# Optimization experiments

Measured on AMD Instinct MI355X. Metric: run time of the kernel, lower is better.

The kernel has to match this reference:

```python
import jax, jax.numpy as jnp
import numpy as np

EPS = 1e-5

def _ln(x, g, b):
    m = jnp.mean(x, -1, keepdims=True)
    v = jnp.var(x, -1, keepdims=True)
    return (x - m) / jnp.sqrt(v + EPS) * g + b

def _rel_shift(x):
    # x: [B, qlen, klen, n_head] -- TransformerXL relative shift
    b, q, k, n = x.shape
    xp = jnp.pad(x, ((0, 0), (0, 0), (1, 0), (0, 0)))  # zero-pad along klen front
    xp = xp.reshape(b, k + 1, q, n)[:, 1:]
    return xp.reshape(b, q, k, n)

def setup_inputs() -> dict:
    key = jax.random.key(0)
    B, Q, D, N, DH, DI = 4, 1024, 1024, 16, 64, 4096
    ks = jax.random.split(key, 9)
    s = 0.02
    w = jax.random.normal(ks[0], (B, Q, D), jnp.float32)
    r = jax.random.normal(ks[1], (1, Q, D), jnp.float32)
    attention_mask = jnp.triu(jnp.ones((Q, Q), bool), k=1)  # 1 == masked (causal)
    qkv_w = jax.random.normal(ks[2], (3 * D, D), jnp.float32) * s
    r_w = jax.random.normal(ks[3], (D, D), jnp.float32) * s
    o_w = jax.random.normal(ks[4], (D, D), jnp.float32) * s
    r_w_bias = jax.random.normal(ks[5], (N, DH), jnp.float32) * s
    r_r_bias = jax.random.normal(ks[6], (N, DH), jnp.float32) * s
    ln1_g = jnp.ones(D, jnp.float32); ln1_b = jnp.zeros(D, jnp.float32)
    ff_w1 = jax.random.normal(ks[7], (DI, D), jnp.float32) * s
    ff_b1 = jnp.zeros(DI, jnp.float32)
    ff_w2 = jax.random.normal(ks[8], (D, DI), jnp.float32) * s
    ff_b2 = jnp.zeros(D, jnp.float32)
    ln2_g = jnp.ones(D, jnp.float32); ln2_b = jnp.zeros(D, jnp.float32)
    return dict(w=w, r=r, attention_mask=attention_mask, qkv_w=qkv_w, r_w=r_w,
                o_w=o_w, r_w_bias=r_w_bias, r_r_bias=r_r_bias, ln1_g=ln1_g,
                ln1_b=ln1_b, ff_w1=ff_w1, ff_b1=ff_b1, ff_w2=ff_w2, ff_b2=ff_b2,
                ln2_g=ln2_g, ln2_b=ln2_b)

def reference(w, r, attention_mask, qkv_w, r_w, o_w, r_w_bias, r_r_bias,
              ln1_g, ln1_b, ff_w1, ff_b1, ff_w2, ff_b2, ln2_g, ln2_b):
    B, Q, D = w.shape
    N, DH = r_w_bias.shape
    # QKV projection (post-lnorm path, no mem)
    heads = w @ qkv_w.T  # [B,Q,3D]
    q, k, v = jnp.split(heads, 3, axis=-1)
    q = q.reshape(B, Q, N, DH)
    k = k.reshape(B, Q, N, DH)
    v = v.reshape(B, Q, N, DH)
    rk = (r[0] @ r_w.T).reshape(Q, N, DH)  # [rlen,N,DH]
    # content (AC) and position (BD) terms, computed in fp32 as in original
    AC = jnp.einsum('bind,bjnd->bijn', q + r_w_bias, k)
    BD = _rel_shift(jnp.einsum('bind,jnd->bijn', q + r_r_bias, rk))
    score = (AC + BD) * (1.0 / jnp.sqrt(jnp.float32(DH)))
    score = jnp.where(attention_mask[None, :, :, None], -1e30, score)
    prob = jax.nn.softmax(score, axis=2)  # softmax over klen
    av = jnp.einsum('bijn,bjnd->bind', prob, v).reshape(B, Q, D)
    out1 = _ln(w + av @ o_w.T, ln1_g, ln1_b)  # deepnorm_alpha = 1.0
    ff = jax.nn.relu(out1 @ ff_w1.T + ff_b1) @ ff_w2.T + ff_b2
    return _ln(out1 + ff, ln2_g, ln2_b)
```

## Files before the change

kernel.cpp:

```cpp
#include <hip/hip_runtime.h>
#include <hip/hip_bf16.h>

typedef __attribute__((ext_vector_type(8))) short short8;
typedef __attribute__((ext_vector_type(4))) short short4v;
typedef __attribute__((ext_vector_type(4))) float floatx4;

__device__ inline float bs2f(short s) {
    unsigned int u = ((unsigned int)(unsigned short)s) << 16;
    float f; __builtin_memcpy(&f, &u, 4); return f;
}
__device__ inline short f2bs(float f) {
    __hip_bfloat16 h = __float2bfloat16(f);
    unsigned short u; __builtin_memcpy(&u, &h, 2); return (short)u;
}
__device__ inline float ldf(const float* p)           { return *p; }
__device__ inline float ldf(const __hip_bfloat16* p)  { return __bfloat162float(*p); }
__device__ inline void  stf(float* p, float v)          { *p = v; }
__device__ inline void  stf(__hip_bfloat16* p, float v) { *p = __float2bfloat16(v); }

__device__ inline void gl_lds16(const short* g, short* l) {
    __builtin_amdgcn_global_load_lds(
        (const __attribute__((address_space(1))) void*)g,
        (__attribute__((address_space(3))) void*)l, 16, 0, 0);
}

__global__ __launch_bounds__(256) void f2b_all_kernel(
    const float* __restrict__ s0, const float* __restrict__ s1,
    const float* __restrict__ s2, const float* __restrict__ s3,
    const float* __restrict__ s4, const float* __restrict__ s5,
    const float* __restrict__ s6, __hip_bfloat16* __restrict__ dst)
{
    const long id  = blockIdx.x;
    const long gid = id * 1024 + threadIdx.x * 4;
    const float* src; long base;
    if      (id < 4096)  { src = s0; base = 0; }
    else if (id < 5120)  { src = s1; base = 4096L  * 1024; }
    else if (id < 8192)  { src = s2; base = 5120L  * 1024; }
    else if (id < 9216)  { src = s3; base = 8192L  * 1024; }
    else if (id < 10240) { src = s4; base = 9216L  * 1024; }
    else if (id < 14336) { src = s5; base = 10240L * 1024; }
    else                 { src = s6; base = 14336L * 1024; }
    const float4 v = *(const float4*)(src + (gid - base));
    dst[gid + 0] = __float2bfloat16(v.x);
    dst[gid + 1] = __float2bfloat16(v.y);
    dst[gid + 2] = __float2bfloat16(v.z);
    dst[gid + 3] = __float2bfloat16(v.w);
}

__global__ __launch_bounds__(256, 2) void gemm128_nt_kernel(
    const __hip_bfloat16* __restrict__ A,
    const __hip_bfloat16* __restrict__ Bw,
    __hip_bfloat16* __restrict__ C,
    int M, int N, int K,
    const float* __restrict__ bias,
    int do_relu)
{
    __shared__ short lA[128 * 32];
    __shared__ short lB[128 * 32];

    const int lane = threadIdx.x & 63;
    const int w    = threadIdx.x >> 6;
    const int m16  = lane & 15;
    const int quad = lane >> 4;
    const int wr   = w >> 1, wc = w & 1;

    const long i0 = (long)blockIdx.y * 128;
    const long j0 = (long)blockIdx.x * 128;

    const short* Ap = (const short*)A;
    const short* Bp = (const short*)Bw;

    floatx4 acc[4][4];
    #pragma unroll
    for (int a = 0; a < 4; ++a)
        #pragma unroll
        for (int b = 0; b < 4; ++b) acc[a][b] = (floatx4){0.f, 0.f, 0.f, 0.f};

    const int srow = w * 32 + (lane >> 2);
    const int scol = (lane & 3) * 8;
    const short* ga = Ap + (i0 + srow) * K + scol;
    const short* gb = Bp + (j0 + srow) * K + scol;
    short* la = lA + (w * 32) * 32;
    short* lb = lB + (w * 32) * 32;

    for (int k0 = 0; k0 < K; k0 += 32) {
        __syncthreads();
        gl_lds16(ga + k0,            la);
        gl_lds16(ga + 16 * K + k0,   la + 16 * 32);
        gl_lds16(gb + k0,            lb);
        gl_lds16(gb + 16 * K + k0,   lb + 16 * 32);
        __syncthreads();

        short8 af[4], bf[4];
        #pragma unroll
        for (int rb = 0; rb < 4; ++rb)
            af[rb] = *(const short8*)&lA[(wr * 64 + rb * 16 + m16) * 32 + quad * 8];
        #pragma unroll
        for (int cb = 0; cb < 4; ++cb)
            bf[cb] = *(const short8*)&lB[(wc * 64 + cb * 16 + m16) * 32 + quad * 8];
        #pragma unroll
        for (int rb = 0; rb < 4; ++rb)
            #pragma unroll
            for (int cb = 0; cb < 4; ++cb)
                acc[rb][cb] = __builtin_amdgcn_mfma_f32_16x16x32_bf16(
                    af[rb], bf[cb], acc[rb][cb], 0, 0, 0);
    }

    #pragma unroll
    for (int cb = 0; cb < 4; ++cb) {
        const long j = j0 + wc * 64 + cb * 16 + m16;
        const float bv = bias ? bias[j] : 0.f;
        #pragma unroll
        for (int rb = 0; rb < 4; ++rb) {
            #pragma unroll
            for (int rr = 0; rr < 4; ++rr) {
                const long row = i0 + wr * 64 + rb * 16 + quad * 4 + rr;
                float v = acc[rb][cb][rr] + bv;
                if (do_relu) v = fmaxf(v, 0.f);
                C[row * N + j] = __float2bfloat16(v);
            }
        }
    }
}

__global__ __launch_bounds__(256, 2) void gemm128_splitk_kernel(
    const __hip_bfloat16* __restrict__ A,
    const __hip_bfloat16* __restrict__ Bw,
    __hip_bfloat16* __restrict__ C0,
    __hip_bfloat16* __restrict__ C1,
    int M, int N, int K)
{
    __shared__ short lA[128 * 32];
    __shared__ short lB[128 * 32];

    const int lane = threadIdx.x & 63;
    const int w    = threadIdx.x >> 6;
    const int m16  = lane & 15;
    const int quad = lane >> 4;
    const int wr   = w >> 1, wc = w & 1;

    const long i0 = (long)blockIdx.y * 128;
    const long j0 = (long)blockIdx.x * 128;
    const int  kz = blockIdx.z;
    const int  kbeg = kz * (K >> 1), kend = kbeg + (K >> 1);

    const short* Ap = (const short*)A;
    const short* Bp = (const short*)Bw;

    floatx4 acc[4][4];
    #pragma unroll
    for (int a = 0; a < 4; ++a)
        #pragma unroll
        for (int b = 0; b < 4; ++b) acc[a][b] = (floatx4){0.f, 0.f, 0.f, 0.f};

    const int srow = w * 32 + (lane >> 2);
    const int scol = (lane & 3) * 8;
    const short* ga = Ap + (i0 + srow) * K + scol;
    const short* gb = Bp + (j0 + srow) * K + scol;
    short* la = lA + (w * 32) * 32;
    short* lb = lB + (w * 32) * 32;

    for (int k0 = kbeg; k0 < kend; k0 += 32) {
        __syncthreads();
        gl_lds16(ga + k0,            la);
        gl_lds16(ga + 16 * K + k0,   la + 16 * 32);
        gl_lds16(gb + k0,            lb);
        gl_lds16(gb + 16 * K + k0,   lb + 16 * 32);
        __syncthreads();

        short8 af[4], bf[4];
        #pragma unroll
        for (int rb = 0; rb < 4; ++rb)
            af[rb] = *(const short8*)&lA[(wr * 64 + rb * 16 + m16) * 32 + quad * 8];
        #pragma unroll
        for (int cb = 0; cb < 4; ++cb)
            bf[cb] = *(const short8*)&lB[(wc * 64 + cb * 16 + m16) * 32 + quad * 8];
        #pragma unroll
        for (int rb = 0; rb < 4; ++rb)
            #pragma unroll
            for (int cb = 0; cb < 4; ++cb)
                acc[rb][cb] = __builtin_amdgcn_mfma_f32_16x16x32_bf16(
                    af[rb], bf[cb], acc[rb][cb], 0, 0, 0);
    }

    __hip_bfloat16* C = kz ? C1 : C0;
    #pragma unroll
    for (int cb = 0; cb < 4; ++cb) {
        const long j = j0 + wc * 64 + cb * 16 + m16;
        #pragma unroll
        for (int rb = 0; rb < 4; ++rb) {
            #pragma unroll
            for (int rr = 0; rr < 4; ++rr) {
                const long row = i0 + wr * 64 + rb * 16 + quad * 4 + rr;
                C[row * N + j] = __float2bfloat16(acc[rb][cb][rr]);
            }
        }
    }
}

__global__ __launch_bounds__(256, 2) void gemm_n64_nt_kernel(
    const __hip_bfloat16* __restrict__ A,
    const __hip_bfloat16* __restrict__ Bw,
    __hip_bfloat16* __restrict__ C,
    int M, int N, int K,
    const float* __restrict__ bias,
    int do_relu)
{
    __shared__ short lA[128 * 32];
    __shared__ short lB[64 * 32];

    const int lane = threadIdx.x & 63;
    const int w    = threadIdx.x >> 6;
    const int m16  = lane & 15;
    const int quad = lane >> 4;
    const int wr   = w >> 1, wc = w & 1;

    const long i0 = (long)blockIdx.y * 128;
    const long j0 = (long)blockIdx.x * 64;

    const short* Ap = (const short*)A;
    const short* Bp = (const short*)Bw;

    floatx4 acc[4][2];
    #pragma unroll
    for (int a = 0; a < 4; ++a)
        #pragma unroll
        for (int b = 0; b < 2; ++b) acc[a][b] = (floatx4){0.f, 0.f, 0.f, 0.f};

    const int srowA = w * 32 + (lane >> 2);
    const int srowB = w * 16 + (lane >> 2);
    const int scol  = (lane & 3) * 8;
    const short* ga = Ap + (i0 + srowA) * K + scol;
    const short* gb = Bp + (j0 + srowB) * K + scol;
    short* la = lA + (w * 32) * 32;
    short* lb = lB + (w * 16) * 32;

    for (int k0 = 0; k0 < K; k0 += 32) {
        __syncthreads();
        gl_lds16(ga + k0,            la);
        gl_lds16(ga + 16 * K + k0,   la + 16 * 32);
        gl_lds16(gb + k0,            lb);
        __syncthreads();

        short8 af[4], bf[2];
        #pragma unroll
        for (int rb = 0; rb < 4; ++rb)
            af[rb] = *(const short8*)&lA[(wr * 64 + rb * 16 + m16) * 32 + quad * 8];
        #pragma unroll
        for (int cb = 0; cb < 2; ++cb)
            bf[cb] = *(const short8*)&lB[(wc * 32 + cb * 16 + m16) * 32 + quad * 8];
        #pragma unroll
        for (int rb = 0; rb < 4; ++rb)
            #pragma unroll
            for (int cb = 0; cb < 2; ++cb)
                acc[rb][cb] = __builtin_amdgcn_mfma_f32_16x16x32_bf16(
                    af[rb], bf[cb], acc[rb][cb], 0, 0, 0);
    }

    #pragma unroll
    for (int cb = 0; cb < 2; ++cb) {
        const long j = j0 + wc * 32 + cb * 16 + m16;
        const float bv = bias ? bias[j] : 0.f;
        #pragma unroll
        for (int rb = 0; rb < 4; ++rb) {
            #pragma unroll
            for (int rr = 0; rr < 4; ++rr) {
                const long row = i0 + wr * 64 + rb * 16 + quad * 4 + rr;
                float v = acc[rb][cb][rr] + bv;
                if (do_relu) v = fmaxf(v, 0.f);
                C[row * N + j] = __float2bfloat16(v);
            }
        }
    }
}

__global__ __launch_bounds__(256) void kvpack_kernel(
    const __hip_bfloat16* __restrict__ heads,
    short* __restrict__ kp, short* __restrict__ vp)
{
    const int Q = 1024, TD = 3072;
    __shared__ short kt[64 * 72];
    __shared__ short vt[64 * 72];
    const int tid = threadIdx.x;
    const int t  = blockIdx.x;
    const int bn = blockIdx.y;
    const int n = bn & 15, b = bn >> 4;
    const int j0 = t * 64;

    const short* hp = (const short*)heads + ((long)(b * Q + j0)) * TD + n * 64;
    {
        const int r = tid >> 2, c0 = (tid & 3) * 16;
        const short* src = hp + (long)r * TD + c0;
        *(short8*)&kt[r * 72 + c0]     = *(const short8*)(src + 1024);
        *(short8*)&kt[r * 72 + c0 + 8] = *(const short8*)(src + 1024 + 8);
        *(short8*)&vt[r * 72 + c0]     = *(const short8*)(src + 2048);
        *(short8*)&vt[r * 72 + c0 + 8] = *(const short8*)(src + 2048 + 8);
    }
    __syncthreads();

    const int lane = tid & 63;
    const int m16 = lane & 15, quad = lane >> 4;
    const long fb = ((long)bn * 16 + t) * 4096;
    #pragma unroll
    for (int pass = 0; pass < 2; ++pass) {
        const int fi = (tid >> 6) + pass * 4;
        const int c = fi >> 2, cb = fi & 3;
        short8 kf = *(const short8*)&kt[(cb * 16 + m16) * 72 + c * 32 + quad * 8];
        *(short8*)(kp + fb + fi * 512 + lane * 8) = kf;
        short8 vf;
        #pragma unroll
        for (int u = 0; u < 8; ++u)
            vf[u] = vt[(c * 32 + quad * 8 + u) * 72 + cb * 16 + m16];
        *(short8*)(vp + fb + fi * 512 + lane * 8) = vf;
    }
}

__global__ __launch_bounds__(256) void rkpack_kernel(
    const __hip_bfloat16* __restrict__ rkb, short* __restrict__ rkp)
{
    const int m = blockIdx.x;
    const int tid = threadIdx.x;
    const short4v v = *(const short4v*)((const short*)rkb + m * 1024 + tid * 4);
    const int n = tid >> 4, d = (tid * 4) & 63;
    *(short4v*)(rkp + ((long)n * 1024 + m) * 64 + d) = v;
}

__global__ __launch_bounds__(256, 2) void fattn_kernel(
    const __hip_bfloat16* __restrict__ heads,
    const short* __restrict__ kp,
    const short* __restrict__ vp,
    const short* __restrict__ rkp,
    const float* __restrict__ rwb,
    const float* __restrict__ rrb,
    __hip_bfloat16* __restrict__ av)
{
    const int Q = 1024, TD = 3072, D = 1024;
    const int tid  = threadIdx.x;
    const int lane = tid & 63;
    const int w    = tid >> 6;
    const int m16  = lane & 15;
    const int quad = lane >> 4;
    const int id = blockIdx.x;
    const int r8 = id & 7;
    const int z  = (id >> 3) & 7;
    const int bn = ((id >> 6) << 3) | r8;
    const int n = bn & 15, b = bn >> 4;

    __shared__ short pbuf[4][16 * 68];
    short* pb = pbuf[w];

    const short* hp = (const short*)heads;

    struct KV { short8 k[8], v[8]; };

    #pragma unroll
    for (int phase = 0; phase < 2; ++phase) {
        const int qt  = phase ? (15 - z) : z;
        const int iw0 = qt * 64 + w * 16;

        short8 qwf[2], qrf[2];
        {
            const long qoff = ((long)(b * Q + iw0 + m16)) * TD + n * 64;
            #pragma unroll
            for (int c = 0; c < 2; ++c) {
                short8 qv = *(const short8*)(hp + qoff + c * 32 + quad * 8);
                #pragma unroll
                for (int u = 0; u < 8; ++u) {
                    const int d = c * 32 + quad * 8 + u;
                    const float f = bs2f(qv[u]);
                    qwf[c][u] = f2bs(f + rwb[n * 64 + d]);
                    qrf[c][u] = f2bs(f + rrb[n * 64 + d]);
                }
            }
        }

        floatx4 oacc[4];
        #pragma unroll
        for (int t = 0; t < 4; ++t) oacc[t] = (floatx4){0.f, 0.f, 0.f, 0.f};
        float lsum[4] = {0.f, 0.f, 0.f, 0.f};

        auto loadKV = [&](KV& f, int t) {
            const long fb = ((long)bn * 16 + t) * 4096 + lane * 8;
            #pragma unroll
            for (int fi = 0; fi < 8; ++fi) {
                f.k[fi] = *(const short8*)(kp + fb + fi * 512);
                f.v[fi] = *(const short8*)(vp + fb + fi * 512);
            }
        };

        auto computeT = [&](const KV& f, int t) {
            const int j0 = t * 64;

            short8 rf[5][2];
            const int m0 = Q - 16 + j0 - iw0;
            #pragma unroll
            for (int cb = 0; cb < 5; ++cb) {
                int m = m0 + cb * 16 + m16;
                if (m > Q - 1) m = Q - 1;
                const long roff = ((long)n * 1024 + m) * 64;
                #pragma unroll
                for (int c = 0; c < 2; ++c)
                    rf[cb][c] = *(const short8*)(rkp + roff + c * 32 + quad * 8);
            }

            floatx4 ac[4];
            #pragma unroll
            for (int cb = 0; cb < 4; ++cb) ac[cb] = (floatx4){0.f, 0.f, 0.f, 0.f};
            #pragma unroll
            for (int c = 0; c < 2; ++c)
                #pragma unroll
                for (int cb = 0; cb < 4; ++cb)
                    ac[cb] = __builtin_amdgcn_mfma_f32_16x16x32_bf16(
                        qwf[c], f.k[c * 4 + cb], ac[cb], 0, 0, 0);

            floatx4 bd[5];
            #pragma unroll
            for (int cb = 0; cb < 5; ++cb) bd[cb] = (floatx4){0.f, 0.f, 0.f, 0.f};
            #pragma unroll
            for (int cb = 0; cb < 5; ++cb)
                #pragma unroll
                for (int c = 0; c < 2; ++c)
                    bd[cb] = __builtin_amdgcn_mfma_f32_16x16x32_bf16(
                        qrf[c], rf[cb][c], bd[cb], 0, 0, 0);

            #pragma unroll
            for (int r = 0; r < 4; ++r) {
                const int ii = quad * 4 + r;
                const int e  = 15 + m16 - ii;
                const int srcLane = (lane & 48) | (e & 15);
                float sh[5];
                #pragma unroll
                for (int cb = 0; cb < 5; ++cb)
                    sh[cb] = __shfl(bd[cb][r], srcLane, 64);
                #pragma unroll
                for (int cb = 0; cb < 4; ++cb) {
                    const float val = (e >= 16) ? sh[cb + 1] : sh[cb];
                    const float sc = (ac[cb][r] + val) * 0.125f;
                    const bool masked = (j0 + cb * 16 + m16) > (iw0 + ii);
                    const float p = masked ? 0.f : __expf(sc);
                    lsum[r] += p;
                    pb[ii * 68 + cb * 16 + m16] = f2bs(p);
                }
            }

            #pragma unroll
            for (int c = 0; c < 2; ++c) {
                const short* pp = pb + m16 * 68 + c * 32 + quad * 8;
                short4v plo = *(const short4v*)pp;
                short4v phi = *(const short4v*)(pp + 4);
                short8 pf;
                #pragma unroll
                for (int u = 0; u < 4; ++u) { pf[u] = plo[u]; pf[u + 4] = phi[u]; }
                #pragma unroll
                for (int cb = 0; cb < 4; ++cb)
                    oacc[cb] = __builtin_amdgcn_mfma_f32_16x16x32_bf16(
                        pf, f.v[c * 4 + cb], oacc[cb], 0, 0, 0);
            }
        };

        KV fa, fb;
        loadKV(fa, 0);
        int t = 0;
        for (;;) {
            if (t < qt) loadKV(fb, t + 1);
            computeT(fa, t);
            if (++t > qt) break;
            if (t < qt) loadKV(fa, t + 1);
            computeT(fb, t);
            if (++t > qt) break;
        }

        #pragma unroll
        for (int r = 0; r < 4; ++r) {
            #pragma unroll
            for (int sft = 1; sft < 16; sft <<= 1)
                lsum[r] += __shfl_xor(lsum[r], sft, 64);
        }
        #pragma unroll
        for (int r = 0; r < 4; ++r) {
            const float linv = 1.f / lsum[r];
            #pragma unroll
            for (int cb = 0; cb < 4; ++cb) {
                const long row = (long)b * Q + iw0 + quad * 4 + r;
                av[row * D + n * 64 + cb * 16 + m16] =
                    __float2bfloat16(oacc[cb][r] * linv);
            }
        }
    }
}

template <typename TA, typename TB, typename TO>
__global__ __launch_bounds__(256) void ln_kernel(
    const TA* __restrict__ xa,
    const TB* __restrict__ xb,
    const float* __restrict__ g,
    const float* __restrict__ beta,
    TO* __restrict__ out)
{
    const int D = 1024;
    const long row = blockIdx.x;
    const int tid = threadIdx.x;
    const TA* pa = xa + row * D;
    const TB* pb = xb + row * D;

    float x[4];
    float s = 0.f, s2 = 0.f;
    #pragma unroll
    for (int u = 0; u < 4; ++u) {
        const int c = tid + u * 256;
        const float v = ldf(pa + c) + ldf(pb + c);
        x[u] = v; s += v; s2 += v * v;
    }
    #pragma unroll
    for (int sft = 32; sft > 0; sft >>= 1) {
        s  += __shfl_xor(s,  sft, 64);
        s2 += __shfl_xor(s2, sft, 64);
    }
    __shared__ float red[8];
    const int wv = tid >> 6, lane = tid & 63;
    if (lane == 0) { red[wv] = s; red[wv + 4] = s2; }
    __syncthreads();
    s  = red[0] + red[1] + red[2] + red[3];
    s2 = red[4] + red[5] + red[6] + red[7];
    const float mean = s * (1.f / D);
    const float var  = s2 * (1.f / D) - mean * mean;
    const float rstd = rsqrtf(var + 1e-5f);
    #pragma unroll
    for (int u = 0; u < 4; ++u) {
        const int c = tid + u * 256;
        const float v = (x[u] - mean) * rstd * g[c] + beta[c];
        stf(out + row * D + c, v);
    }
}

template <typename TA, typename TO>
__global__ __launch_bounds__(256) void ln3_kernel(
    const TA* __restrict__ xa,
    const __hip_bfloat16* __restrict__ p0,
    const __hip_bfloat16* __restrict__ p1,
    const float* __restrict__ bias,
    const float* __restrict__ g,
    const float* __restrict__ beta,
    TO* __restrict__ out)
{
    const int D = 1024;
    const long row = blockIdx.x;
    const int tid = threadIdx.x;
    const TA* pa = xa + row * D;
    const __hip_bfloat16* q0 = p0 + row * D;
    const __hip_bfloat16* q1 = p1 + row * D;

    float x[4];
    float s = 0.f, s2 = 0.f;
    #pragma unroll
    for (int u = 0; u < 4; ++u) {
        const int c = tid + u * 256;
        float v = ldf(pa + c) + ldf(q0 + c) + ldf(q1 + c);
        if (bias) v += bias[c];
        x[u] = v; s += v; s2 += v * v;
    }
    #pragma unroll
    for (int sft = 32; sft > 0; sft >>= 1) {
        s  += __shfl_xor(s,  sft, 64);
        s2 += __shfl_xor(s2, sft, 64);
    }
    __shared__ float red[8];
    const int wv = tid >> 6, lane = tid & 63;
    if (lane == 0) { red[wv] = s; red[wv + 4] = s2; }
    __syncthreads();
    s  = red[0] + red[1] + red[2] + red[3];
    s2 = red[4] + red[5] + red[6] + red[7];
    const float mean = s * (1.f / D);
    const float var  = s2 * (1.f / D) - mean * mean;
    const float rstd = rsqrtf(var + 1e-5f);
    #pragma unroll
    for (int u = 0; u < 4; ++u) {
        const int c = tid + u * 256;
        const float v = (x[u] - mean) * rstd * g[c] + beta[c];
        stf(out + row * D + c, v);
    }
}

extern "C" void kernel_launch(void* const* d_in, const int* in_sizes, int n_in,
                              void* d_out, int out_size, void* d_ws, size_t ws_size,
                              hipStream_t stream)
{
    const int B = 4, Q = 1024, D = 1024, N = 16, TD = 3072, DI = 4096;
    const int BQ = B * Q;

    const float* w     = (const float*)d_in[0];
    const float* r     = (const float*)d_in[1];
    const float* qkv_w = (const float*)d_in[3];
    const float* r_w   = (const float*)d_in[4];
    const float* o_w   = (const float*)d_in[5];
    const float* rwb   = (const float*)d_in[6];
    const float* rrb   = (const float*)d_in[7];
    const float* ln1g  = (const float*)d_in[8];
    const float* ln1b  = (const float*)d_in[9];
    const float* ffw1  = (const float*)d_in[10];
    const float* ffb1  = (const float*)d_in[11];
    const float* ffw2  = (const float*)d_in[12];
    const float* ffb2  = (const float*)d_in[13];
    const float* ln2g  = (const float*)d_in[14];
    const float* ln2b  = (const float*)d_in[15];
    float* out = (float*)d_out;

    __hip_bfloat16* wsb   = (__hip_bfloat16*)d_ws;
    __hip_bfloat16* heads = wsb;
    __hip_bfloat16* rkb   = heads + (long)BQ * TD;
    __hip_bfloat16* av    = rkb   + (long)Q * D;
    __hip_bfloat16* ffh   = wsb;
    __hip_bfloat16* oproj = av    + (long)BQ * D;
    __hip_bfloat16* out1  = oproj + (long)BQ * D;
    __hip_bfloat16* cvt   = out1  + (long)BQ * D;
    __hip_bfloat16* wb    = cvt;
    __hip_bfloat16* rb    = wb    + (long)BQ * D;
    __hip_bfloat16* qkvwb = rb    + (long)Q * D;
    __hip_bfloat16* rwwb  = qkvwb + (long)TD * D;
    __hip_bfloat16* owb   = rwwb  + (long)D * D;
    __hip_bfloat16* f1wb  = owb   + (long)D * D;
    __hip_bfloat16* f2wb  = f1wb  + (long)DI * D;
    short* kp  = (short*)wb;
    short* vpk = (short*)rb;
    short* rkp = (short*)rwwb;
    __hip_bfloat16* part0 = wb;
    __hip_bfloat16* part1 = wb + (long)BQ * D;

    const dim3 blk(256);

    f2b_all_kernel<<<dim3(18432), blk, 0, stream>>>(
        w, r, qkv_w, r_w, o_w, ffw1, ffw2, wb);

    gemm128_nt_kernel<<<dim3(TD / 128, BQ / 128), blk, 0, stream>>>(
        wb, qkvwb, heads, BQ, TD, D, nullptr, 0);
    gemm_n64_nt_kernel<<<dim3(D / 64, Q / 128), blk, 0, stream>>>(
        rb, rwwb, rkb, Q, D, D, nullptr, 0);
    kvpack_kernel<<<dim3(16, B * N), blk, 0, stream>>>(heads, kp, vpk);
    rkpack_kernel<<<dim3(Q), blk, 0, stream>>>(rkb, rkp);
    fattn_kernel<<<dim3(512), blk, 0, stream>>>(
        heads, kp, vpk, rkp, rwb, rrb, av);
    gemm128_splitk_kernel<<<dim3(D / 128, BQ / 128, 2), blk, 0, stream>>>(
        av, owb, part0, part1, BQ, D, D);
    ln3_kernel<float, __hip_bfloat16>
        <<<dim3(BQ), blk, 0, stream>>>(w, part0, part1, nullptr, ln1g, ln1b, out1);
    gemm128_nt_kernel<<<dim3(DI / 128, BQ / 128), blk, 0, stream>>>(
        out1, f1wb, ffh, BQ, DI, D, ffb1, 1);
    gemm128_splitk_kernel<<<dim3(D / 128, BQ / 128, 2), blk, 0, stream>>>(
        ffh, f2wb, part0, part1, BQ, D, DI);
    ln3_kernel<__hip_bfloat16, float>
        <<<dim3(BQ), blk, 0, stream>>>(out1, part0, part1, ffb2, ln2g, ln2b, out);
}
```

Before: 395.7 us.

## Merge QKV/rk GEMMs and pack kernels, split-K by four for FF2, stage attention output

The QKV projection and the rk projection now run in a single launch, with extra column blocks handling rk, and the kv pack and rk pack kernels are merged into one. The FF2 GEMM is split four ways along K, and a new layernorm kernel sums four partial buffers. The attention epilogue first stages its output in LDS and then writes coalesced 16-byte rows. The aim is fewer launches, better CU occupancy on the long-K GEMM and fewer narrow global stores. The cost is more partial-sum traffic for FF2 and some idle blocks in the merged grid.

```diff
diff --git a/kernel.cpp b/kernel.cpp
--- a/kernel.cpp
+++ b/kernel.cpp
@@ -47,28 +47,17 @@
     dst[gid + 3] = __float2bfloat16(v.w);
 }
 
-__global__ __launch_bounds__(256, 2) void gemm128_nt_kernel(
-    const __hip_bfloat16* __restrict__ A,
-    const __hip_bfloat16* __restrict__ Bw,
-    __hip_bfloat16* __restrict__ C,
-    int M, int N, int K,
-    const float* __restrict__ bias,
-    int do_relu)
-{
-    __shared__ short lA[128 * 32];
-    __shared__ short lB[128 * 32];
-
+__device__ __forceinline__ void gemm128_body(
+    const short* __restrict__ Ap, const short* __restrict__ Bp,
+    __hip_bfloat16* __restrict__ C, int N, int K, long i0, long j0,
+    int kbeg, int kend, const float* __restrict__ bias, int do_relu,
+    short* lA, short* lB)
+{
     const int lane = threadIdx.x & 63;
     const int w    = threadIdx.x >> 6;
     const int m16  = lane & 15;
     const int quad = lane >> 4;
     const int wr   = w >> 1, wc = w & 1;
-
-    const long i0 = (long)blockIdx.y * 128;
-    const long j0 = (long)blockIdx.x * 128;
-
-    const short* Ap = (const short*)A;
-    const short* Bp = (const short*)Bw;
 
     floatx4 acc[4][4];
     #pragma unroll
@@ -83,7 +72,7 @@
     short* la = lA + (w * 32) * 32;
     short* lb = lB + (w * 32) * 32;
 
-    for (int k0 = 0; k0 < K; k0 += 32) {
+    for (int k0 = kbeg; k0 < kend; k0 += 32) {
         __syncthreads();
         gl_lds16(ga + k0,            la);
         gl_lds16(ga + 16 * K + k0,   la + 16 * 32);
@@ -123,165 +112,91 @@
     }
 }
 
-__global__ __launch_bounds__(256, 2) void gemm128_splitk_kernel(
+__global__ __launch_bounds__(256, 2) void gemm128_nt_kernel(
+    const __hip_bfloat16* __restrict__ A,
+    const __hip_bfloat16* __restrict__ Bw,
+    __hip_bfloat16* __restrict__ C,
+    int N, int K,
+    const float* __restrict__ bias,
+    int do_relu)
+{
+    __shared__ short lA[128 * 32];
+    __shared__ short lB[128 * 32];
+    gemm128_body((const short*)A, (const short*)Bw, C, N, K,
+                 (long)blockIdx.y * 128, (long)blockIdx.x * 128,
+                 0, K, bias, do_relu, lA, lB);
+}
+
+__global__ __launch_bounds__(256, 2) void qkv_rkb_kernel(
+    const __hip_bfloat16* __restrict__ wb,
+    const __hip_bfloat16* __restrict__ qkvwb,
+    __hip_bfloat16* __restrict__ heads,
+    const __hip_bfloat16* __restrict__ rb,
+    const __hip_bfloat16* __restrict__ rwwb,
+    __hip_bfloat16* __restrict__ rkb)
+{
+    __shared__ short lA[128 * 32];
+    __shared__ short lB[128 * 32];
+    if (blockIdx.x < 24) {
+        gemm128_body((const short*)wb, (const short*)qkvwb, heads, 3072, 1024,
+                     (long)blockIdx.y * 128, (long)blockIdx.x * 128,
+                     0, 1024, nullptr, 0, lA, lB);
+    } else {
+        if (blockIdx.y >= 8) return;
+        gemm128_body((const short*)rb, (const short*)rwwb, rkb, 1024, 1024,
+                     (long)blockIdx.y * 128, (long)(blockIdx.x - 24) * 128,
+                     0, 1024, nullptr, 0, lA, lB);
+    }
+}
+
+__global__ __launch_bounds__(256, 2) void gemm128_sk2_kernel(
     const __hip_bfloat16* __restrict__ A,
     const __hip_bfloat16* __restrict__ Bw,
     __hip_bfloat16* __restrict__ C0,
     __hip_bfloat16* __restrict__ C1,
-    int M, int N, int K)
+    int N, int K)
 {
     __shared__ short lA[128 * 32];
     __shared__ short lB[128 * 32];
-
-    const int lane = threadIdx.x & 63;
-    const int w    = threadIdx.x >> 6;
-    const int m16  = lane & 15;
-    const int quad = lane >> 4;
-    const int wr   = w >> 1, wc = w & 1;
-
-    const long i0 = (long)blockIdx.y * 128;
-    const long j0 = (long)blockIdx.x * 128;
-    const int  kz = blockIdx.z;
-    const int  kbeg = kz * (K >> 1), kend = kbeg + (K >> 1);
-
-    const short* Ap = (const short*)A;
-    const short* Bp = (const short*)Bw;
-
-    floatx4 acc[4][4];
-    #pragma unroll
-    for (int a = 0; a < 4; ++a)
-        #pragma unroll
-        for (int b = 0; b < 4; ++b) acc[a][b] = (floatx4){0.f, 0.f, 0.f, 0.f};
-
-    const int srow = w * 32 + (lane >> 2);
-    const int scol = (lane & 3) * 8;
-    const short* ga = Ap + (i0 + srow) * K + scol;
-    const short* gb = Bp + (j0 + srow) * K + scol;
-    short* la = lA + (w * 32) * 32;
-    short* lb = lB + (w * 32) * 32;
-
-    for (int k0 = kbeg; k0 < kend; k0 += 32) {
-        __syncthreads();
-        gl_lds16(ga + k0,            la);
-        gl_lds16(ga + 16 * K + k0,   la + 16 * 32);
-        gl_lds16(gb + k0,            lb);
-        gl_lds16(gb + 16 * K + k0,   lb + 16 * 32);
-        __syncthreads();
-
-        short8 af[4], bf[4];
-        #pragma unroll
-        for (int rb = 0; rb < 4; ++rb)
-            af[rb] = *(const short8*)&lA[(wr * 64 + rb * 16 + m16) * 32 + quad * 8];
-        #pragma unroll
-        for (int cb = 0; cb < 4; ++cb)
-            bf[cb] = *(const short8*)&lB[(wc * 64 + cb * 16 + m16) * 32 + quad * 8];
-        #pragma unroll
-        for (int rb = 0; rb < 4; ++rb)
-            #pragma unroll
-            for (int cb = 0; cb < 4; ++cb)
-                acc[rb][cb] = __builtin_amdgcn_mfma_f32_16x16x32_bf16(
-                    af[rb], bf[cb], acc[rb][cb], 0, 0, 0);
-    }
-
-    __hip_bfloat16* C = kz ? C1 : C0;
-    #pragma unroll
-    for (int cb = 0; cb < 4; ++cb) {
-        const long j = j0 + wc * 64 + cb * 16 + m16;
-        #pragma unroll
-        for (int rb = 0; rb < 4; ++rb) {
-            #pragma unroll
-            for (int rr = 0; rr < 4; ++rr) {
-                const long row = i0 + wr * 64 + rb * 16 + quad * 4 + rr;
-                C[row * N + j] = __float2bfloat16(acc[rb][cb][rr]);
-            }
-        }
-    }
-}
-
-__global__ __launch_bounds__(256, 2) void gemm_n64_nt_kernel(
+    const int kz = blockIdx.z;
+    gemm128_body((const short*)A, (const short*)Bw, kz ? C1 : C0, N, K,
+                 (long)blockIdx.y * 128, (long)blockIdx.x * 128,
+                 kz * (K >> 1), kz * (K >> 1) + (K >> 1), nullptr, 0, lA, lB);
+}
+
+__global__ __launch_bounds__(256, 2) void gemm128_sk4_kernel(
     const __hip_bfloat16* __restrict__ A,
     const __hip_bfloat16* __restrict__ Bw,
-    __hip_bfloat16* __restrict__ C,
-    int M, int N, int K,
-    const float* __restrict__ bias,
-    int do_relu)
+    __hip_bfloat16* __restrict__ C0, __hip_bfloat16* __restrict__ C1,
+    __hip_bfloat16* __restrict__ C2, __hip_bfloat16* __restrict__ C3,
+    int N, int K)
 {
     __shared__ short lA[128 * 32];
-    __shared__ short lB[64 * 32];
-
-    const int lane = threadIdx.x & 63;
-    const int w    = threadIdx.x >> 6;
-    const int m16  = lane & 15;
-    const int quad = lane >> 4;
-    const int wr   = w >> 1, wc = w & 1;
-
-    const long i0 = (long)blockIdx.y * 128;
-    const long j0 = (long)blockIdx.x * 64;
-
-    const short* Ap = (const short*)A;
-    const short* Bp = (const short*)Bw;
-
-    floatx4 acc[4][2];
-    #pragma unroll
-    for (int a = 0; a < 4; ++a)
-        #pragma unroll
-        for (int b = 0; b < 2; ++b) acc[a][b] = (floatx4){0.f, 0.f, 0.f, 0.f};
-
-    const int srowA = w * 32 + (lane >> 2);
-    const int srowB = w * 16 + (lane >> 2);
-    const int scol  = (lane & 3) * 8;
-    const short* ga = Ap + (i0 + srowA) * K + scol;
-    const short* gb = Bp + (j0 + srowB) * K + scol;
-    short* la = lA + (w * 32) * 32;
-    short* lb = lB + (w * 16) * 32;
-
-    for (int k0 = 0; k0 < K; k0 += 32) {
-        __syncthreads();
-        gl_lds16(ga + k0,            la);
-        gl_lds16(ga + 16 * K + k0,   la + 16 * 32);
-        gl_lds16(gb + k0,            lb);
-        __syncthreads();
-
-        short8 af[4], bf[2];
-        #pragma unroll
-        for (int rb = 0; rb < 4; ++rb)
-            af[rb] = *(const short8*)&lA[(wr * 64 + rb * 16 + m16) * 32 + quad * 8];
-        #pragma unroll
-        for (int cb = 0; cb < 2; ++cb)
-            bf[cb] = *(const short8*)&lB[(wc * 32 + cb * 16 + m16) * 32 + quad * 8];
-        #pragma unroll
-        for (int rb = 0; rb < 4; ++rb)
-            #pragma unroll
-            for (int cb = 0; cb < 2; ++cb)
-                acc[rb][cb] = __builtin_amdgcn_mfma_f32_16x16x32_bf16(
-                    af[rb], bf[cb], acc[rb][cb], 0, 0, 0);
-    }
-
-    #pragma unroll
-    for (int cb = 0; cb < 2; ++cb) {
-        const long j = j0 + wc * 32 + cb * 16 + m16;
-        const float bv = bias ? bias[j] : 0.f;
-        #pragma unroll
-        for (int rb = 0; rb < 4; ++rb) {
-            #pragma unroll
-            for (int rr = 0; rr < 4; ++rr) {
-                const long row = i0 + wr * 64 + rb * 16 + quad * 4 + rr;
-                float v = acc[rb][cb][rr] + bv;
-                if (do_relu) v = fmaxf(v, 0.f);
-                C[row * N + j] = __float2bfloat16(v);
-            }
-        }
-    }
-}
-
-__global__ __launch_bounds__(256) void kvpack_kernel(
+    __shared__ short lB[128 * 32];
+    const int kz = blockIdx.z;
+    __hip_bfloat16* C = (kz == 0) ? C0 : (kz == 1) ? C1 : (kz == 2) ? C2 : C3;
+    const int kq = K >> 2;
+    gemm128_body((const short*)A, (const short*)Bw, C, N, K,
+                 (long)blockIdx.y * 128, (long)blockIdx.x * 128,
+                 kz * kq, kz * kq + kq, nullptr, 0, lA, lB);
+}
+
+__global__ __launch_bounds__(256) void pack_kernel(
     const __hip_bfloat16* __restrict__ heads,
-    short* __restrict__ kp, short* __restrict__ vp)
+    const __hip_bfloat16* __restrict__ rkb,
+    short* __restrict__ kp, short* __restrict__ vp, short* __restrict__ rkp)
 {
     const int Q = 1024, TD = 3072;
+    const int tid = threadIdx.x;
+    if (blockIdx.x >= 16) {
+        const int m = (blockIdx.x - 16) * 64 + blockIdx.y;
+        const short4v v = *(const short4v*)((const short*)rkb + m * 1024 + tid * 4);
+        const int n = tid >> 4, d = (tid * 4) & 63;
+        *(short4v*)(rkp + ((long)n * 1024 + m) * 64 + d) = v;
+        return;
+    }
     __shared__ short kt[64 * 72];
     __shared__ short vt[64 * 72];
-    const int tid = threadIdx.x;
     const int t  = blockIdx.x;
     const int bn = blockIdx.y;
     const int n = bn & 15, b = bn >> 4;
@@ -313,16 +228,6 @@
             vf[u] = vt[(c * 32 + quad * 8 + u) * 72 + cb * 16 + m16];
         *(short8*)(vp + fb + fi * 512 + lane * 8) = vf;
     }
-}
-
-__global__ __launch_bounds__(256) void rkpack_kernel(
-    const __hip_bfloat16* __restrict__ rkb, short* __restrict__ rkp)
-{
-    const int m = blockIdx.x;
-    const int tid = threadIdx.x;
-    const short4v v = *(const short4v*)((const short*)rkb + m * 1024 + tid * 4);
-    const int n = tid >> 4, d = (tid * 4) & 63;
-    *(short4v*)(rkp + ((long)n * 1024 + m) * 64 + d) = v;
 }
 
 __global__ __launch_bounds__(256, 2) void fattn_kernel(
@@ -399,19 +304,19 @@
                 if (m > Q - 1) m = Q - 1;
                 const long roff = ((long)n * 1024 + m) * 64;
                 #pragma unroll
-                for (int c = 0; c < 2; ++c)
-                    rf[cb][c] = *(const short8*)(rkp + roff + c * 32 + quad * 8);
+                for (int cc = 0; cc < 2; ++cc)
+                    rf[cb][cc] = *(const short8*)(rkp + roff + cc * 32 + quad * 8);
             }
 
             floatx4 ac[4];
             #pragma unroll
             for (int cb = 0; cb < 4; ++cb) ac[cb] = (floatx4){0.f, 0.f, 0.f, 0.f};
             #pragma unroll
-            for (int c = 0; c < 2; ++c)
+            for (int cc = 0; cc < 2; ++cc)
                 #pragma unroll
                 for (int cb = 0; cb < 4; ++cb)
                     ac[cb] = __builtin_amdgcn_mfma_f32_16x16x32_bf16(
-                        qwf[c], f.k[c * 4 + cb], ac[cb], 0, 0, 0);
+                        qwf[cc], f.k[cc * 4 + cb], ac[cb], 0, 0, 0);
 
             floatx4 bd[5];
             #pragma unroll
@@ -419,9 +324,9 @@
             #pragma unroll
             for (int cb = 0; cb < 5; ++cb)
                 #pragma unroll
-                for (int c = 0; c < 2; ++c)
+                for (int cc = 0; cc < 2; ++cc)
                     bd[cb] = __builtin_amdgcn_mfma_f32_16x16x32_bf16(
-                        qrf[c], rf[cb][c], bd[cb], 0, 0, 0);
+                        qrf[cc], rf[cb][cc], bd[cb], 0, 0, 0);
 
             #pragma unroll
             for (int r = 0; r < 4; ++r) {
@@ -444,8 +349,8 @@
             }
 
             #pragma unroll
-            for (int c = 0; c < 2; ++c) {
-                const short* pp = pb + m16 * 68 + c * 32 + quad * 8;
+            for (int cc = 0; cc < 2; ++cc) {
+                const short* pp = pb + m16 * 68 + cc * 32 + quad * 8;
                 short4v plo = *(const short4v*)pp;
                 short4v phi = *(const short4v*)(pp + 4);
                 short8 pf;
@@ -454,7 +359,7 @@
                 #pragma unroll
                 for (int cb = 0; cb < 4; ++cb)
                     oacc[cb] = __builtin_amdgcn_mfma_f32_16x16x32_bf16(
-                        pf, f.v[c * 4 + cb], oacc[cb], 0, 0, 0);
+                        pf, f.v[cc * 4 + cb], oacc[cb], 0, 0, 0);
             }
         };
 
@@ -479,20 +384,27 @@
         #pragma unroll
         for (int r = 0; r < 4; ++r) {
             const float linv = 1.f / lsum[r];
-            #pragma unroll
-            for (int cb = 0; cb < 4; ++cb) {
-                const long row = (long)b * Q + iw0 + quad * 4 + r;
-                av[row * D + n * 64 + cb * 16 + m16] =
-                    __float2bfloat16(oacc[cb][r] * linv);
-            }
+            const int ii = quad * 4 + r;
+            #pragma unroll
+            for (int cb = 0; cb < 4; ++cb)
+                pb[ii * 64 + cb * 16 + m16] = f2bs(oacc[cb][r] * linv);
         }
-    }
-}
-
-template <typename TA, typename TB, typename TO>
-__global__ __launch_bounds__(256) void ln_kernel(
+        #pragma unroll
+        for (int u = 0; u < 2; ++u) {
+            const int rr = u * 8 + (lane >> 3);
+            const int cc = (lane & 7) * 8;
+            short8 o = *(const short8*)&pb[rr * 64 + cc];
+            *(short8*)((short*)av + ((long)b * Q + iw0 + rr) * D + n * 64 + cc) = o;
+        }
+    }
+}
+
+template <typename TA, typename TO>
+__global__ __launch_bounds__(256) void ln3_kernel(
     const TA* __restrict__ xa,
-    const TB* __restrict__ xb,
+    const __hip_bfloat16* __restrict__ p0,
+    const __hip_bfloat16* __restrict__ p1,
+    const float* __restrict__ bias,
     const float* __restrict__ g,
     const float* __restrict__ beta,
     TO* __restrict__ out)
@@ -501,14 +413,16 @@
     const long row = blockIdx.x;
     const int tid = threadIdx.x;
     const TA* pa = xa + row * D;
-    const TB* pb = xb + row * D;
+    const __hip_bfloat16* q0 = p0 + row * D;
+    const __hip_bfloat16* q1 = p1 + row * D;
 
     float x[4];
     float s = 0.f, s2 = 0.f;
     #pragma unroll
     for (int u = 0; u < 4; ++u) {
         const int c = tid + u * 256;
-        const float v = ldf(pa + c) + ldf(pb + c);
+        float v = ldf(pa + c) + ldf(q0 + c) + ldf(q1 + c);
+        if (bias) v += bias[c];
         x[u] = v; s += v; s2 += v * v;
     }
     #pragma unroll
@@ -534,10 +448,12 @@
 }
 
 template <typename TA, typename TO>
-__global__ __launch_bounds__(256) void ln3_kernel(
+__global__ __launch_bounds__(256) void ln5_kernel(
     const TA* __restrict__ xa,
     const __hip_bfloat16* __restrict__ p0,
     const __hip_bfloat16* __restrict__ p1,
+    const __hip_bfloat16* __restrict__ p2,
+    const __hip_bfloat16* __restrict__ p3,
     const float* __restrict__ bias,
     const float* __restrict__ g,
     const float* __restrict__ beta,
@@ -549,13 +465,16 @@
     const TA* pa = xa + row * D;
     const __hip_bfloat16* q0 = p0 + row * D;
     const __hip_bfloat16* q1 = p1 + row * D;
+    const __hip_bfloat16* q2 = p2 + row * D;
+    const __hip_bfloat16* q3 = p3 + row * D;
 
     float x[4];
     float s = 0.f, s2 = 0.f;
     #pragma unroll
     for (int u = 0; u < 4; ++u) {
         const int c = tid + u * 256;
-        float v = ldf(pa + c) + ldf(q0 + c) + ldf(q1 + c);
+        float v = ldf(pa + c) + ldf(q0 + c) + ldf(q1 + c)
+                + ldf(q2 + c) + ldf(q3 + c);
         if (bias) v += bias[c];
         x[u] = v; s += v; s2 += v * v;
     }
@@ -625,28 +544,28 @@
     short* rkp = (short*)rwwb;
     __hip_bfloat16* part0 = wb;
     __hip_bfloat16* part1 = wb + (long)BQ * D;
+    __hip_bfloat16* part2 = wb + 2L * BQ * D;
+    __hip_bfloat16* part3 = oproj;
 
     const dim3 blk(256);
 
     f2b_all_kernel<<<dim3(18432), blk, 0, stream>>>(
         w, r, qkv_w, r_w, o_w, ffw1, ffw2, wb);
 
-    gemm128_nt_kernel<<<dim3(TD / 128, BQ / 128), blk, 0, stream>>>(
-        wb, qkvwb, heads, BQ, TD, D, nullptr, 0);
-    gemm_n64_nt_kernel<<<dim3(D / 64, Q / 128), blk, 0, stream>>>(
-        rb, rwwb, rkb, Q, D, D, nullptr, 0);
-    kvpack_kernel<<<dim3(16, B * N), blk, 0, stream>>>(heads, kp, vpk);
-    rkpack_kernel<<<dim3(Q), blk, 0, stream>>>(rkb, rkp);
+    qkv_rkb_kernel<<<dim3(32, 32), blk, 0, stream>>>(
+        wb, qkvwb, heads, rb, rwwb, rkb);
+    pack_kernel<<<dim3(32, B * N), blk, 0, stream>>>(heads, rkb, kp, vpk, rkp);
     fattn_kernel<<<dim3(512), blk, 0, stream>>>(
         heads, kp, vpk, rkp, rwb, rrb, av);
-    gemm128_splitk_kernel<<<dim3(D / 128, BQ / 128, 2), blk, 0, stream>>>(
-        av, owb, part0, part1, BQ, D, D);
+    gemm128_sk2_kernel<<<dim3(D / 128, BQ / 128, 2), blk, 0, stream>>>(
+        av, owb, part0, part1, D, D);
     ln3_kernel<float, __hip_bfloat16>
         <<<dim3(BQ), blk, 0, stream>>>(w, part0, part1, nullptr, ln1g, ln1b, out1);
     gemm128_nt_kernel<<<dim3(DI / 128, BQ / 128), blk, 0, stream>>>(
-        out1, f1wb, ffh, BQ, DI, D, ffb1, 1);
-    gemm128_splitk_kernel<<<dim3(D / 128, BQ / 128, 2), blk, 0, stream>>>(
-        ffh, f2wb, part0, part1, BQ, D, DI);
-    ln3_kernel<__hip_bfloat16, float>
-        <<<dim3(BQ), blk, 0, stream>>>(out1, part0, part1, ffb2, ln2g, ln2b, out);
-}
+        out1, f1wb, ffh, DI, D, ffb1, 1);
+    gemm128_sk4_kernel<<<dim3(D / 128, BQ / 128, 4), blk, 0, stream>>>(
+        ffh, f2wb, part0, part1, part2, part3, D, DI);
+    ln5_kernel<__hip_bfloat16, float>
+        <<<dim3(BQ), blk, 0, stream>>>(out1, part0, part1, part2, part3,
+                                       ffb2, ln2g, ln2b, out);
+}
```

After: 389.3 us. About the same (-1.6%).
